# Performance work log

Hardware: AMD Instinct MI355X
Metric: run time of the kernel (lower is better)

## Reference

```python
import jax, jax.numpy as jnp
import numpy as np

N_QUBITS = 4
Q_LAYERS = 3
BATCH = 16384


def setup_inputs() -> dict:
    key = jax.random.key(0)
    ks = jax.random.split(key, 12)

    def n(k, shape, s=0.1):
        return (s * jax.random.normal(k, shape)).astype(jnp.float32)

    return {
        "x": jax.random.normal(ks[0], (BATCH, 1, 28, 28), jnp.float32),
        "conv1_w": n(ks[1], (6, 1, 5, 5)),
        "conv1_b": n(ks[2], (6,)),
        "conv2_w": n(ks[3], (16, 6, 5, 5)),
        "conv2_b": n(ks[4], (16,)),
        "fc1_w": n(ks[5], (120, 256)),
        "fc1_b": n(ks[6], (120,)),
        "fc2_w": n(ks[7], (N_QUBITS, 120)),
        "fc2_b": n(ks[8], (N_QUBITS,)),
        "q_weights": n(ks[9], (Q_LAYERS, 1, N_QUBITS, 3), 0.01),
        "clf_w": n(ks[10], (10, N_QUBITS)),
        "clf_b": n(ks[11], (10,)),
    }


def _apply_1q(state, U, w):
    # state: (B, 2,2,2,2); U: (2,2) shared or (B,2,2) per-sample
    s = jnp.moveaxis(state, 1 + w, -1)
    if U.ndim == 2:
        s = jnp.einsum('ij,...j->...i', U, s)
    else:
        s = jnp.einsum('bij,b...j->b...i', U, s)
    return jnp.moveaxis(s, -1, 1 + w)


def _cnot(state, c, t):
    s = jnp.moveaxis(state, (1 + c, 1 + t), (-2, -1))
    s = jnp.concatenate([s[..., 0:1, :], s[..., 1:2, ::-1]], axis=-2)
    return jnp.moveaxis(s, (-2, -1), (1 + c, 1 + t))


def _rot(phi, theta, omega):
    # PennyLane Rot = RZ(omega) @ RY(theta) @ RZ(phi)
    c = jnp.cos(theta / 2)
    s = jnp.sin(theta / 2)
    m00 = jnp.exp(-0.5j * (phi + omega)) * c
    m01 = -jnp.exp(0.5j * (phi - omega)) * s
    m10 = jnp.exp(0.5j * (omega - phi)) * s
    m11 = jnp.exp(0.5j * (phi + omega)) * c
    return jnp.stack([jnp.stack([m00, m01]), jnp.stack([m10, m11])])


def _rx(a):
    # a: (B,) -> (B,2,2) RX matrices
    c = jnp.cos(a / 2) + 0j
    z = -1j * jnp.sin(a / 2)
    return jnp.stack([jnp.stack([c, z], -1), jnp.stack([z, c], -1)], -2)


def _circuit(angles, qw):
    # Data-reuploading circuit: per block, StronglyEntanglingLayers(1 sublayer, r=1)
    # then AngleEmbedding (RX). Returns <Z_i> per qubit, shape (B, 4).
    Bn = angles.shape[0]
    state = jnp.zeros((Bn, 16), jnp.complex64).at[:, 0].set(1.0)
    state = state.reshape(Bn, 2, 2, 2, 2)
    n_layers = qw.shape[0]
    for l in range(n_layers):
        for w in range(N_QUBITS):
            state = _apply_1q(state, _rot(qw[l, 0, w, 0], qw[l, 0, w, 1], qw[l, 0, w, 2]), w)
        for w in range(N_QUBITS):
            state = _cnot(state, w, (w + 1) % N_QUBITS)
        for w in range(N_QUBITS):
            state = _apply_1q(state, _rx(angles[:, w]), w)
    probs = jnp.abs(state) ** 2
    z = []
    for w in range(N_QUBITS):
        p = jnp.moveaxis(probs, 1 + w, -1).reshape(Bn, -1, 2)
        z.append(p[..., 0].sum(-1) - p[..., 1].sum(-1))
    return jnp.stack(z, axis=1).astype(jnp.float32)


def _conv(x, w, b):
    y = jax.lax.conv_general_dilated(x, w, (1, 1), 'VALID',
                                     dimension_numbers=('NCHW', 'OIHW', 'NCHW'))
    return y + b[None, :, None, None]


def _pool(x):
    return jax.lax.reduce_window(x, -jnp.inf, jax.lax.max,
                                 (1, 1, 2, 2), (1, 1, 2, 2), 'VALID')


def reference(x, conv1_w, conv1_b, conv2_w, conv2_b, fc1_w, fc1_b,
              fc2_w, fc2_b, q_weights, clf_w, clf_b):
    h = _pool(jax.nn.relu(_conv(x, conv1_w, conv1_b)))       # (B,6,12,12)
    h = _pool(jax.nn.relu(_conv(h, conv2_w, conv2_b)))       # (B,16,4,4)
    h = h.reshape(h.shape[0], -1)                            # (B,256)
    h = jax.nn.relu(h @ fc1_w.T + fc1_b)                     # (B,120)
    feat = h @ fc2_w.T + fc2_b                               # (B,4)
    angles = jnp.pi * jax.nn.sigmoid(feat)
    q_out = _circuit(angles, q_weights)                      # (B,4)
    logits = q_out @ clf_w.T + clf_b                         # (B,10)
    return logits
```

## Files before the change

kernel.cpp:

```cpp
#include <hip/hip_runtime.h>
#include <math.h>

#define BATCH_N 16384

typedef _Float16 half8 __attribute__((ext_vector_type(8)));
typedef __fp16 h2 __attribute__((ext_vector_type(2)));
typedef float f32x4 __attribute__((ext_vector_type(4)));

#define C1P_F  0
#define BS1_F  120
#define BS2_F  128
#define FC2W_F 144
#define ROTM_F 628
#define RXCS_F 724
#define CWB_F  852
#define W2B_F  904
#define PW_F   2760
#define LDS_FLOATS 9768

#define WV_STRIDE_H 3504
#define H1_SAMP 1240
#define H2_OFF  2480

__global__ __launch_bounds__(256, 4) void fused_model(
    const float* __restrict__ xg,
    const float* __restrict__ c1w, const float* __restrict__ c1b,
    const float* __restrict__ c2w, const float* __restrict__ c2b,
    const float* __restrict__ f1w, const float* __restrict__ f1b,
    const float* __restrict__ f2w, const float* __restrict__ f2b,
    const float* __restrict__ qw,  const float* __restrict__ cw,
    const float* __restrict__ cbias, float* __restrict__ out) {
    __shared__ float L[LDS_FLOATS];
    const int tid = threadIdx.x;
    const int b0 = blockIdx.x * 16;
    const int lane = tid & 63, wvi = tid >> 6;
    const int ml = lane & 15, q = lane >> 4;

    _Float16* W2BH = (_Float16*)(L + W2B_F);
    _Float16* PWH  = (_Float16*)(L + PW_F);
    _Float16* H1CH = PWH + wvi * WV_STRIDE_H;
    _Float16* H2H  = H1CH + H2_OFF;
    _Float16* HSH  = (_Float16*)(L + W2B_F);

    if (tid < 120) {
        const int oc = tid / 20, r = tid - oc * 20, ky = r >> 2, j = r & 3;
        const float* wb = c1w + oc * 25 + ky * 5;
        float lo, hi;
        if (j == 0)      { lo = wb[0]; hi = wb[1]; }
        else if (j == 1) { lo = wb[2]; hi = wb[3]; }
        else if (j == 2) { lo = wb[4]; hi = 0.f;   }
        else             { lo = 0.f;   hi = wb[4]; }
        ((h2*)&L[C1P_F])[tid] = __builtin_amdgcn_cvt_pkrtz(lo, hi);
    }
    if (tid < 6)  L[BS1_F + tid] = c1b[tid];
    if (tid < 16) L[BS2_F + tid] = c2b[tid];
    for (int i = tid; i < 480; i += 256) L[FC2W_F + i] = f2w[i];
    if (tid < 4) L[FC2W_F + 480 + tid] = f2b[tid];
    if (tid < 40) L[CWB_F + tid] = cw[tid];
    if (tid < 10) L[CWB_F + 40 + tid] = cbias[tid];
    if (tid < 12) {
        const float phi = qw[tid * 3 + 0];
        const float th  = qw[tid * 3 + 1];
        const float om  = qw[tid * 3 + 2];
        const float ct = cosf(0.5f * th), st = sinf(0.5f * th);
        const float ap = 0.5f * (phi + om), bm = 0.5f * (phi - om);
        const float ca = cosf(ap), sa = sinf(ap);
        const float cbm = cosf(bm), sbm = sinf(bm);
        float* R = &L[ROTM_F + tid * 8];
        R[0] =  ct * ca;  R[1] = -ct * sa;
        R[2] = -st * cbm; R[3] = -st * sbm;
        R[4] =  st * cbm; R[5] = -st * sbm;
        R[6] =  ct * ca;  R[7] =  ct * sa;
    }
    for (int i = tid; i < 3712; i += 256) {
        const int oc = i / 232, r = i - oc * 232;
        float v = 0.f;
        if (r < 200) {
            const int pix = r >> 3, ic = r & 7;
            if (ic < 6) v = c2w[oc * 150 + ic * 25 + pix];
        }
        W2BH[oc * 232 + r] = (_Float16)v;
    }
    __syncthreads();

#pragma unroll 1
    for (int p = 0; p < 2; ++p) {
        const int sbase = b0 + 4 * wvi + 2 * p;

        for (int t = lane; t < 288; t += 64) {
            const int s = t >= 144 ? 1 : 0;
            const int r = t - s * 144;
            const int py = r / 12, px = r - (r / 12) * 12;
            const float* xp = xg + (size_t)(sbase + s) * 784 + (2 * py) * 28 + 2 * px;

            float4 X4[6]; float2 X2[6];
#pragma unroll
            for (int rr = 0; rr < 6; rr++) {
                X4[rr] = *(const float4*)(xp + rr * 28);
                X2[rr] = *(const float2*)(xp + rr * 28 + 4);
            }

            float acc[6][4];
#pragma unroll
            for (int oc = 0; oc < 6; oc++) {
                const float bv = L[BS1_F + oc];
                acc[oc][0] = bv; acc[oc][1] = bv; acc[oc][2] = bv; acc[oc][3] = bv;
            }

            h2 R0[5], R1[5];
            R0[0] = __builtin_amdgcn_cvt_pkrtz(X4[0].x, X4[0].y);
            R0[1] = __builtin_amdgcn_cvt_pkrtz(X4[0].z, X4[0].w);
            R0[2] = __builtin_amdgcn_cvt_pkrtz(X2[0].x, X2[0].y);
            R0[3] = __builtin_amdgcn_cvt_pkrtz(X4[0].y, X4[0].z);
            R0[4] = __builtin_amdgcn_cvt_pkrtz(X4[0].w, X2[0].x);
#pragma unroll
            for (int ky = 0; ky < 5; ky++) {
                R1[0] = __builtin_amdgcn_cvt_pkrtz(X4[ky + 1].x, X4[ky + 1].y);
                R1[1] = __builtin_amdgcn_cvt_pkrtz(X4[ky + 1].z, X4[ky + 1].w);
                R1[2] = __builtin_amdgcn_cvt_pkrtz(X2[ky + 1].x, X2[ky + 1].y);
                R1[3] = __builtin_amdgcn_cvt_pkrtz(X4[ky + 1].y, X4[ky + 1].z);
                R1[4] = __builtin_amdgcn_cvt_pkrtz(X4[ky + 1].w, X2[ky + 1].x);
#pragma unroll
                for (int oc = 0; oc < 6; oc++) {
                    union { uint4 v; h2 h[4]; } W;
                    W.v = ((const uint4*)&L[C1P_F])[oc * 5 + ky];
                    acc[oc][0] = __builtin_amdgcn_fdot2(R0[0], W.h[0], acc[oc][0], false);
                    acc[oc][0] = __builtin_amdgcn_fdot2(R0[1], W.h[1], acc[oc][0], false);
                    acc[oc][0] = __builtin_amdgcn_fdot2(R0[2], W.h[2], acc[oc][0], false);
                    acc[oc][1] = __builtin_amdgcn_fdot2(R0[3], W.h[0], acc[oc][1], false);
                    acc[oc][1] = __builtin_amdgcn_fdot2(R0[4], W.h[1], acc[oc][1], false);
                    acc[oc][1] = __builtin_amdgcn_fdot2(R0[2], W.h[3], acc[oc][1], false);
                    acc[oc][2] = __builtin_amdgcn_fdot2(R1[0], W.h[0], acc[oc][2], false);
                    acc[oc][2] = __builtin_amdgcn_fdot2(R1[1], W.h[1], acc[oc][2], false);
                    acc[oc][2] = __builtin_amdgcn_fdot2(R1[2], W.h[2], acc[oc][2], false);
                    acc[oc][3] = __builtin_amdgcn_fdot2(R1[3], W.h[0], acc[oc][3], false);
                    acc[oc][3] = __builtin_amdgcn_fdot2(R1[4], W.h[1], acc[oc][3], false);
                    acc[oc][3] = __builtin_amdgcn_fdot2(R1[2], W.h[3], acc[oc][3], false);
                }
#pragma unroll
                for (int j = 0; j < 5; j++) R0[j] = R1[j];
            }

            union { _Float16 h[8]; uint4 u; } O;
#pragma unroll
            for (int oc = 0; oc < 6; oc++) {
                const float m = fmaxf(fmaxf(acc[oc][0], acc[oc][1]), fmaxf(acc[oc][2], acc[oc][3]));
                O.h[oc] = (_Float16)fmaxf(m, 0.f);
            }
            O.h[6] = (_Float16)0.f; O.h[7] = (_Float16)0.f;
            *(uint4*)(H1CH + s * H1_SAMP + (py * 13 + px) * 8) = O.u;
        }
        __builtin_amdgcn_wave_barrier();

        {
            f32x4 c2a[2][4];
#pragma unroll
            for (int a = 0; a < 2; a++)
#pragma unroll
                for (int b = 0; b < 4; b++) c2a[a][b] = (f32x4){0.f, 0.f, 0.f, 0.f};

#pragma unroll
            for (int ks = 0; ks < 7; ks++) {
                const half8 bfrag = *(const half8*)(W2BH + ml * 232 + ks * 32 + q * 8);
                int tp = ks * 4 + q; if (tp > 24) tp = 24;
                const int poff = (tp / 5) * 13 + (tp % 5);
#pragma unroll
                for (int si = 0; si < 2; si++) {
                    const _Float16* hp = H1CH + si * H1_SAMP;
#pragma unroll
                    for (int t = 0; t < 4; t++) {
                        const int cp = t * 16 + ml;
                        const int unit = (cp >> 3) * 13 + (cp & 7) + poff;
                        const half8 afrag = *(const half8*)(hp + unit * 8);
                        c2a[si][t] = __builtin_amdgcn_mfma_f32_16x16x32_f16(afrag, bfrag, c2a[si][t], 0, 0, 0);
                    }
                }
            }

            const float bv = L[BS2_F + ml];
#pragma unroll
            for (int si = 0; si < 2; si++) {
#pragma unroll
                for (int t = 0; t < 4; t++) {
                    const float c0 = c2a[si][t][0] + bv, c1 = c2a[si][t][1] + bv;
                    const float c2 = c2a[si][t][2] + bv, c3 = c2a[si][t][3] + bv;
                    float px0 = fmaxf(c0, c1), px1 = fmaxf(c2, c3);
                    px0 = fmaxf(px0, __shfl_xor(px0, 32));
                    px1 = fmaxf(px1, __shfl_xor(px1, 32));
                    if (lane < 32) {
                        union { _Float16 h[2]; unsigned u; } P2;
                        P2.h[0] = (_Float16)fmaxf(px0, 0.f);
                        P2.h[1] = (_Float16)fmaxf(px1, 0.f);
                        *(unsigned*)(H2H + (2 * p + si) * 256 + ml * 16 + t * 4 + (q & 1) * 2) = P2.u;
                    }
                }
            }
        }
        __builtin_amdgcn_wave_barrier();
    }
    __syncthreads();

    {
        f32x4 fcC[2];
        fcC[0] = (f32x4){0.f, 0.f, 0.f, 0.f};
        fcC[1] = (f32x4){0.f, 0.f, 0.f, 0.f};
        const _Float16* h2p = PWH + (ml >> 2) * WV_STRIDE_H + H2_OFF + (ml & 3) * 256;
#pragma unroll
        for (int ks = 0; ks < 8; ks++) {
            const half8 afrag = *(const half8*)(h2p + ks * 32 + q * 8);
#pragma unroll
            for (int ti = 0; ti < 2; ti++) {
                const int n = (wvi + 4 * ti) * 16 + ml;
                half8 bfrag;
                if (n < 120) {
                    const float* wp = f1w + (size_t)n * 256 + ks * 32 + q * 8;
                    const float4 u = *(const float4*)wp;
                    const float4 v = *(const float4*)(wp + 4);
                    bfrag[0] = (_Float16)u.x; bfrag[1] = (_Float16)u.y;
                    bfrag[2] = (_Float16)u.z; bfrag[3] = (_Float16)u.w;
                    bfrag[4] = (_Float16)v.x; bfrag[5] = (_Float16)v.y;
                    bfrag[6] = (_Float16)v.z; bfrag[7] = (_Float16)v.w;
                } else {
#pragma unroll
                    for (int j = 0; j < 8; j++) bfrag[j] = (_Float16)0.f;
                }
                fcC[ti] = __builtin_amdgcn_mfma_f32_16x16x32_f16(afrag, bfrag, fcC[ti], 0, 0, 0);
            }
        }
#pragma unroll
        for (int ti = 0; ti < 2; ti++) {
            const int n = (wvi + 4 * ti) * 16 + ml;
            if (n < 120) {
                const float bb = f1b[n];
#pragma unroll
                for (int rg = 0; rg < 4; rg++) {
                    const int s = q * 4 + rg;
                    HSH[s * 128 + n] = (_Float16)fmaxf(fcC[ti][rg] + bb, 0.f);
                }
            }
        }
    }
    __syncthreads();

    if (tid < 64) {
        const int s = tid >> 2, m = tid & 3;
        float f = L[FC2W_F + 480 + m];
        for (int nn = 0; nn < 120; nn += 8) {
            const half8 hv = *(const half8*)(HSH + s * 128 + nn);
            const float* wp = &L[FC2W_F + m * 120 + nn];
            f = fmaf(wp[0], (float)hv[0], f); f = fmaf(wp[1], (float)hv[1], f);
            f = fmaf(wp[2], (float)hv[2], f); f = fmaf(wp[3], (float)hv[3], f);
            f = fmaf(wp[4], (float)hv[4], f); f = fmaf(wp[5], (float)hv[5], f);
            f = fmaf(wp[6], (float)hv[6], f); f = fmaf(wp[7], (float)hv[7], f);
        }
        const float ang = 3.14159265358979323846f / (1.f + expf(-f));
        L[RXCS_F + tid]      = cosf(0.5f * ang);
        L[RXCS_F + 64 + tid] = sinf(0.5f * ang);
    }
    __syncthreads();

    {
        const int s = tid >> 4, a = tid & 15;
        float ar = (a == 0) ? 1.f : 0.f, ai = 0.f;

#pragma unroll
        for (int l = 0; l < 3; l++) {
#pragma unroll
            for (int w = 0; w < 4; w++) {
                const float* R = &L[ROTM_F + (l * 4 + w) * 8];
                const int mask = 8 >> w;
                const float pr = __shfl_xor(ar, mask);
                const float pi = __shfl_xor(ai, mask);
                const bool bit = (a & mask) != 0;
                const float lr = bit ? pr : ar, li = bit ? pi : ai;
                const float hr = bit ? ar : pr, hi = bit ? ai : pi;
                const float Ar = bit ? R[4] : R[0], Ai = bit ? R[5] : R[1];
                const float Br = bit ? R[6] : R[2], Bi = bit ? R[7] : R[3];
                ar = Ar * lr - Ai * li + Br * hr - Bi * hi;
                ai = Ar * li + Ai * lr + Br * hi + Bi * hr;
            }
#pragma unroll
            for (int w = 0; w < 4; w++) {
                const int mc = 8 >> w, mt = 8 >> ((w + 1) & 3);
                const float pr = __shfl_xor(ar, mt);
                const float pi = __shfl_xor(ai, mt);
                const bool ctrl = (a & mc) != 0;
                ar = ctrl ? pr : ar;
                ai = ctrl ? pi : ai;
            }
#pragma unroll
            for (int w = 0; w < 4; w++) {
                const int mask = 8 >> w;
                const float c  = L[RXCS_F + s * 4 + w];
                const float s2 = L[RXCS_F + 64 + s * 4 + w];
                const float pr = __shfl_xor(ar, mask);
                const float pi = __shfl_xor(ai, mask);
                const float nr = fmaf(c, ar, s2 * pi);
                const float ni = fmaf(c, ai, -s2 * pr);
                ar = nr; ai = ni;
            }
        }

        float v = ar * ar + ai * ai;
#pragma unroll
        for (int d = 1; d < 16; d <<= 1) {
            const float pv = __shfl_xor(v, d);
            v = (a & d) ? (pv - v) : (v + pv);
        }

        if (a < 10) {
            const int base = (tid & 63) & ~15;
            float lg = L[CWB_F + 40 + a];
#pragma unroll
            for (int w = 0; w < 4; w++) {
                const float zw = __shfl(v, base | (8 >> w));
                lg = fmaf(L[CWB_F + a * 4 + w], zw, lg);
            }
            out[(size_t)(b0 + s) * 10 + a] = lg;
        }
    }
}

extern "C" void kernel_launch(void* const* d_in, const int* in_sizes, int n_in,
                              void* d_out, int out_size, void* d_ws, size_t ws_size,
                              hipStream_t stream) {
    const float* x   = (const float*)d_in[0];
    const float* c1w = (const float*)d_in[1];
    const float* c1b = (const float*)d_in[2];
    const float* c2w = (const float*)d_in[3];
    const float* c2b = (const float*)d_in[4];
    const float* f1w = (const float*)d_in[5];
    const float* f1b = (const float*)d_in[6];
    const float* f2w = (const float*)d_in[7];
    const float* f2b = (const float*)d_in[8];
    const float* qw  = (const float*)d_in[9];
    const float* cw  = (const float*)d_in[10];
    const float* cb  = (const float*)d_in[11];
    float* out = (float*)d_out;

    fused_model<<<BATCH_N / 16, 256, 0, stream>>>(x, c1w, c1b, c2w, c2b,
                                                  f1w, f1b, f2w, f2b,
                                                  qw, cw, cb, out);
}
```

Before: 157.3 us.

## Stage input tile in LDS as fp16, hold pooled conv2 in registers, spread fc2

Each wave now loads its two 28x28 input images once, coalesced, into LDS as packed fp16. The conv1 taps are then read from LDS with shifted unsigned words, replacing six overlapping float4/float2 global loads per thread. Pooled conv2 outputs stay in registers until a block barrier and are then written to a compact shared A-matrix for fc1. fc2 is split across all 256 threads with shuffle reductions and reads its weights directly from global memory. Other changes include incremental index math for the conv2 weight staging, packed fp16 conversions for the fc1 weights, and a reorganised LDS layout. The cost is a larger LDS footprint and more registers, which may reduce occupancy.

```diff
diff --git a/kernel.cpp b/kernel.cpp
--- a/kernel.cpp
+++ b/kernel.cpp
@@ -10,17 +10,34 @@
 #define C1P_F  0
 #define BS1_F  120
 #define BS2_F  128
-#define FC2W_F 144
-#define ROTM_F 628
-#define RXCS_F 724
-#define CWB_F  852
-#define W2B_F  904
-#define PW_F   2760
-#define LDS_FLOATS 9768
-
-#define WV_STRIDE_H 3504
-#define H1_SAMP 1240
-#define H2_OFF  2480
+#define ROTM_F 144
+#define RXCS_F 240
+#define CWB_F  368
+#define W2B_F  420
+#define PW_F   2276
+#define LDS_FLOATS 10020
+
+#define WV_STRIDE_H 3872
+#define XH_SAMP_H   784
+#define H1_OFF_H    1568
+#define H1_SAMP_H   1152
+#define H2A_ROW_H   264
+#define HS_OFF_H    4224
+#define HS_ROW_H    136
+
+static __device__ __forceinline__ h2 u2h(unsigned u) {
+    union { unsigned u; h2 h; } c; c.u = u; return c.h;
+}
+
+struct Row5 { h2 a0, a1, a2, s0, s1; };
+static __device__ __forceinline__ Row5 ldrow(const unsigned* xw) {
+    const unsigned u0 = xw[0], u1 = xw[1], u2 = xw[2];
+    Row5 r;
+    r.a0 = u2h(u0); r.a1 = u2h(u1); r.a2 = u2h(u2);
+    r.s0 = u2h((u0 >> 16) | (u1 << 16));
+    r.s1 = u2h((u1 >> 16) | (u2 << 16));
+    return r;
+}
 
 __global__ __launch_bounds__(256, 4) void fused_model(
     const float* __restrict__ xg,
@@ -38,9 +55,10 @@
 
     _Float16* W2BH = (_Float16*)(L + W2B_F);
     _Float16* PWH  = (_Float16*)(L + PW_F);
-    _Float16* H1CH = PWH + wvi * WV_STRIDE_H;
-    _Float16* H2H  = H1CH + H2_OFF;
-    _Float16* HSH  = (_Float16*)(L + W2B_F);
+    _Float16* XHH  = PWH + wvi * WV_STRIDE_H;
+    _Float16* H1CH = XHH + H1_OFF_H;
+    _Float16* H2AH = PWH;
+    _Float16* HSH  = PWH + HS_OFF_H;
 
     if (tid < 120) {
         const int oc = tid / 20, r = tid - oc * 20, ky = r >> 2, j = r & 3;
@@ -54,8 +72,6 @@
     }
     if (tid < 6)  L[BS1_F + tid] = c1b[tid];
     if (tid < 16) L[BS2_F + tid] = c2b[tid];
-    for (int i = tid; i < 480; i += 256) L[FC2W_F + i] = f2w[i];
-    if (tid < 4) L[FC2W_F + 480 + tid] = f2b[tid];
     if (tid < 40) L[CWB_F + tid] = cw[tid];
     if (tid < 10) L[CWB_F + 40 + tid] = cbias[tid];
     if (tid < 12) {
@@ -72,33 +88,46 @@
         R[4] =  st * cbm; R[5] = -st * sbm;
         R[6] =  ct * ca;  R[7] =  ct * sa;
     }
-    for (int i = tid; i < 3712; i += 256) {
-        const int oc = i / 232, r = i - oc * 232;
-        float v = 0.f;
-        if (r < 200) {
-            const int pix = r >> 3, ic = r & 7;
-            if (ic < 6) v = c2w[oc * 150 + ic * 25 + pix];
-        }
-        W2BH[oc * 232 + r] = (_Float16)v;
-    }
-    __syncthreads();
-
+    {
+        int oc = (tid >= 232) ? 1 : 0;
+        int r = tid - oc * 232;
 #pragma unroll 1
+        for (int i = tid; i < 3712; i += 256) {
+            float v = 0.f;
+            if (r < 200) {
+                const int pix = r >> 3, ic = r & 7;
+                if (ic < 6) v = c2w[oc * 150 + ic * 25 + pix];
+            }
+            W2BH[oc * 232 + r] = (_Float16)v;
+            r += 24; oc += 1;
+            if (r >= 232) { r -= 232; oc += 1; }
+        }
+    }
+    __syncthreads();
+
+    unsigned h2r[2][2][4];
+
+#pragma unroll 2
     for (int p = 0; p < 2; ++p) {
         const int sbase = b0 + 4 * wvi + 2 * p;
+
+        for (int k = lane; k < 392; k += 64) {
+            const int s = (k >= 196) ? 1 : 0;
+            const int kk = k - 196 * s;
+            const int row = kk / 7, q4 = kk - row * 7;
+            const float4 v = *(const float4*)(xg + (size_t)(sbase + s) * 784 + row * 28 + q4 * 4);
+            union { h2 h[2]; uint2 u; } W;
+            W.h[0] = __builtin_amdgcn_cvt_pkrtz(v.x, v.y);
+            W.h[1] = __builtin_amdgcn_cvt_pkrtz(v.z, v.w);
+            *(uint2*)(XHH + s * XH_SAMP_H + row * 28 + q4 * 4) = W.u;
+        }
+        __builtin_amdgcn_wave_barrier();
 
         for (int t = lane; t < 288; t += 64) {
             const int s = t >= 144 ? 1 : 0;
             const int r = t - s * 144;
             const int py = r / 12, px = r - (r / 12) * 12;
-            const float* xp = xg + (size_t)(sbase + s) * 784 + (2 * py) * 28 + 2 * px;
-
-            float4 X4[6]; float2 X2[6];
-#pragma unroll
-            for (int rr = 0; rr < 6; rr++) {
-                X4[rr] = *(const float4*)(xp + rr * 28);
-                X2[rr] = *(const float2*)(xp + rr * 28 + 4);
-            }
+            const unsigned* xw = (const unsigned*)(XHH + s * XH_SAMP_H) + 2 * py * 14 + px;
 
             float acc[6][4];
 #pragma unroll
@@ -107,38 +136,28 @@
                 acc[oc][0] = bv; acc[oc][1] = bv; acc[oc][2] = bv; acc[oc][3] = bv;
             }
 
-            h2 R0[5], R1[5];
-            R0[0] = __builtin_amdgcn_cvt_pkrtz(X4[0].x, X4[0].y);
-            R0[1] = __builtin_amdgcn_cvt_pkrtz(X4[0].z, X4[0].w);
-            R0[2] = __builtin_amdgcn_cvt_pkrtz(X2[0].x, X2[0].y);
-            R0[3] = __builtin_amdgcn_cvt_pkrtz(X4[0].y, X4[0].z);
-            R0[4] = __builtin_amdgcn_cvt_pkrtz(X4[0].w, X2[0].x);
+            Row5 R0 = ldrow(xw);
 #pragma unroll
             for (int ky = 0; ky < 5; ky++) {
-                R1[0] = __builtin_amdgcn_cvt_pkrtz(X4[ky + 1].x, X4[ky + 1].y);
-                R1[1] = __builtin_amdgcn_cvt_pkrtz(X4[ky + 1].z, X4[ky + 1].w);
-                R1[2] = __builtin_amdgcn_cvt_pkrtz(X2[ky + 1].x, X2[ky + 1].y);
-                R1[3] = __builtin_amdgcn_cvt_pkrtz(X4[ky + 1].y, X4[ky + 1].z);
-                R1[4] = __builtin_amdgcn_cvt_pkrtz(X4[ky + 1].w, X2[ky + 1].x);
+                const Row5 R1 = ldrow(xw + (ky + 1) * 14);
 #pragma unroll
                 for (int oc = 0; oc < 6; oc++) {
                     union { uint4 v; h2 h[4]; } W;
                     W.v = ((const uint4*)&L[C1P_F])[oc * 5 + ky];
-                    acc[oc][0] = __builtin_amdgcn_fdot2(R0[0], W.h[0], acc[oc][0], false);
-                    acc[oc][0] = __builtin_amdgcn_fdot2(R0[1], W.h[1], acc[oc][0], false);
-                    acc[oc][0] = __builtin_amdgcn_fdot2(R0[2], W.h[2], acc[oc][0], false);
-                    acc[oc][1] = __builtin_amdgcn_fdot2(R0[3], W.h[0], acc[oc][1], false);
-                    acc[oc][1] = __builtin_amdgcn_fdot2(R0[4], W.h[1], acc[oc][1], false);
-                    acc[oc][1] = __builtin_amdgcn_fdot2(R0[2], W.h[3], acc[oc][1], false);
-                    acc[oc][2] = __builtin_amdgcn_fdot2(R1[0], W.h[0], acc[oc][2], false);
-                    acc[oc][2] = __builtin_amdgcn_fdot2(R1[1], W.h[1], acc[oc][2], false);
-                    acc[oc][2] = __builtin_amdgcn_fdot2(R1[2], W.h[2], acc[oc][2], false);
-                    acc[oc][3] = __builtin_amdgcn_fdot2(R1[3], W.h[0], acc[oc][3], false);
-                    acc[oc][3] = __builtin_amdgcn_fdot2(R1[4], W.h[1], acc[oc][3], false);
-                    acc[oc][3] = __builtin_amdgcn_fdot2(R1[2], W.h[3], acc[oc][3], false);
-                }
-#pragma unroll
-                for (int j = 0; j < 5; j++) R0[j] = R1[j];
+                    acc[oc][0] = __builtin_amdgcn_fdot2(R0.a0, W.h[0], acc[oc][0], false);
+                    acc[oc][0] = __builtin_amdgcn_fdot2(R0.a1, W.h[1], acc[oc][0], false);
+                    acc[oc][0] = __builtin_amdgcn_fdot2(R0.a2, W.h[2], acc[oc][0], false);
+                    acc[oc][1] = __builtin_amdgcn_fdot2(R0.s0, W.h[0], acc[oc][1], false);
+                    acc[oc][1] = __builtin_amdgcn_fdot2(R0.s1, W.h[1], acc[oc][1], false);
+                    acc[oc][1] = __builtin_amdgcn_fdot2(R0.a2, W.h[3], acc[oc][1], false);
+                    acc[oc][2] = __builtin_amdgcn_fdot2(R1.a0, W.h[0], acc[oc][2], false);
+                    acc[oc][2] = __builtin_amdgcn_fdot2(R1.a1, W.h[1], acc[oc][2], false);
+                    acc[oc][2] = __builtin_amdgcn_fdot2(R1.a2, W.h[2], acc[oc][2], false);
+                    acc[oc][3] = __builtin_amdgcn_fdot2(R1.s0, W.h[0], acc[oc][3], false);
+                    acc[oc][3] = __builtin_amdgcn_fdot2(R1.s1, W.h[1], acc[oc][3], false);
+                    acc[oc][3] = __builtin_amdgcn_fdot2(R1.a2, W.h[3], acc[oc][3], false);
+                }
+                R0 = R1;
             }
 
             union { _Float16 h[8]; uint4 u; } O;
@@ -148,7 +167,7 @@
                 O.h[oc] = (_Float16)fmaxf(m, 0.f);
             }
             O.h[6] = (_Float16)0.f; O.h[7] = (_Float16)0.f;
-            *(uint4*)(H1CH + s * H1_SAMP + (py * 13 + px) * 8) = O.u;
+            *(uint4*)(H1CH + s * H1_SAMP_H + (py * 12 + px) * 8) = O.u;
         }
         __builtin_amdgcn_wave_barrier();
 
@@ -163,14 +182,14 @@
             for (int ks = 0; ks < 7; ks++) {
                 const half8 bfrag = *(const half8*)(W2BH + ml * 232 + ks * 32 + q * 8);
                 int tp = ks * 4 + q; if (tp > 24) tp = 24;
-                const int poff = (tp / 5) * 13 + (tp % 5);
+                const int poff = (tp / 5) * 12 + (tp % 5);
 #pragma unroll
                 for (int si = 0; si < 2; si++) {
-                    const _Float16* hp = H1CH + si * H1_SAMP;
+                    const _Float16* hp = H1CH + si * H1_SAMP_H;
 #pragma unroll
                     for (int t = 0; t < 4; t++) {
                         const int cp = t * 16 + ml;
-                        const int unit = (cp >> 3) * 13 + (cp & 7) + poff;
+                        const int unit = (cp >> 3) * 12 + (cp & 7) + poff;
                         const half8 afrag = *(const half8*)(hp + unit * 8);
                         c2a[si][t] = __builtin_amdgcn_mfma_f32_16x16x32_f16(afrag, bfrag, c2a[si][t], 0, 0, 0);
                     }
@@ -187,16 +206,27 @@
                     float px0 = fmaxf(c0, c1), px1 = fmaxf(c2, c3);
                     px0 = fmaxf(px0, __shfl_xor(px0, 32));
                     px1 = fmaxf(px1, __shfl_xor(px1, 32));
-                    if (lane < 32) {
-                        union { _Float16 h[2]; unsigned u; } P2;
-                        P2.h[0] = (_Float16)fmaxf(px0, 0.f);
-                        P2.h[1] = (_Float16)fmaxf(px1, 0.f);
-                        *(unsigned*)(H2H + (2 * p + si) * 256 + ml * 16 + t * 4 + (q & 1) * 2) = P2.u;
-                    }
+                    union { _Float16 h[2]; unsigned u; } P2;
+                    P2.h[0] = (_Float16)fmaxf(px0, 0.f);
+                    P2.h[1] = (_Float16)fmaxf(px1, 0.f);
+                    h2r[p][si][t] = P2.u;
                 }
             }
         }
         __builtin_amdgcn_wave_barrier();
+    }
+    __syncthreads();
+
+    if (lane < 32) {
+#pragma unroll
+        for (int p = 0; p < 2; p++)
+#pragma unroll
+            for (int si = 0; si < 2; si++)
+#pragma unroll
+                for (int t = 0; t < 4; t++) {
+                    const int srow = 4 * wvi + 2 * p + si;
+                    *(unsigned*)(H2AH + srow * H2A_ROW_H + ml * 16 + t * 4 + q * 2) = h2r[p][si][t];
+                }
     }
     __syncthreads();
 
@@ -204,7 +234,7 @@
         f32x4 fcC[2];
         fcC[0] = (f32x4){0.f, 0.f, 0.f, 0.f};
         fcC[1] = (f32x4){0.f, 0.f, 0.f, 0.f};
-        const _Float16* h2p = PWH + (ml >> 2) * WV_STRIDE_H + H2_OFF + (ml & 3) * 256;
+        const _Float16* h2p = H2AH + ml * H2A_ROW_H;
 #pragma unroll
         for (int ks = 0; ks < 8; ks++) {
             const half8 afrag = *(const half8*)(h2p + ks * 32 + q * 8);
@@ -216,10 +246,12 @@
                     const float* wp = f1w + (size_t)n * 256 + ks * 32 + q * 8;
                     const float4 u = *(const float4*)wp;
                     const float4 v = *(const float4*)(wp + 4);
-                    bfrag[0] = (_Float16)u.x; bfrag[1] = (_Float16)u.y;
-                    bfrag[2] = (_Float16)u.z; bfrag[3] = (_Float16)u.w;
-                    bfrag[4] = (_Float16)v.x; bfrag[5] = (_Float16)v.y;
-                    bfrag[6] = (_Float16)v.z; bfrag[7] = (_Float16)v.w;
+                    union { h2 p[4]; half8 h8; } B;
+                    B.p[0] = __builtin_amdgcn_cvt_pkrtz(u.x, u.y);
+                    B.p[1] = __builtin_amdgcn_cvt_pkrtz(u.z, u.w);
+                    B.p[2] = __builtin_amdgcn_cvt_pkrtz(v.x, v.y);
+                    B.p[3] = __builtin_amdgcn_cvt_pkrtz(v.z, v.w);
+                    bfrag = B.h8;
                 } else {
 #pragma unroll
                     for (int j = 0; j < 8; j++) bfrag[j] = (_Float16)0.f;
@@ -235,27 +267,37 @@
 #pragma unroll
                 for (int rg = 0; rg < 4; rg++) {
                     const int s = q * 4 + rg;
-                    HSH[s * 128 + n] = (_Float16)fmaxf(fcC[ti][rg] + bb, 0.f);
-                }
-            }
-        }
-    }
-    __syncthreads();
-
-    if (tid < 64) {
-        const int s = tid >> 2, m = tid & 3;
-        float f = L[FC2W_F + 480 + m];
-        for (int nn = 0; nn < 120; nn += 8) {
-            const half8 hv = *(const half8*)(HSH + s * 128 + nn);
-            const float* wp = &L[FC2W_F + m * 120 + nn];
-            f = fmaf(wp[0], (float)hv[0], f); f = fmaf(wp[1], (float)hv[1], f);
-            f = fmaf(wp[2], (float)hv[2], f); f = fmaf(wp[3], (float)hv[3], f);
-            f = fmaf(wp[4], (float)hv[4], f); f = fmaf(wp[5], (float)hv[5], f);
-            f = fmaf(wp[6], (float)hv[6], f); f = fmaf(wp[7], (float)hv[7], f);
-        }
-        const float ang = 3.14159265358979323846f / (1.f + expf(-f));
-        L[RXCS_F + tid]      = cosf(0.5f * ang);
-        L[RXCS_F + 64 + tid] = sinf(0.5f * ang);
+                    HSH[s * HS_ROW_H + n] = (_Float16)fmaxf(fcC[ti][rg] + bb, 0.f);
+                }
+            }
+        }
+    }
+    __syncthreads();
+
+    {
+        const int s = tid >> 4, m = (tid >> 2) & 3, part = tid & 3;
+        float f = (part == 0) ? f2b[m] : 0.f;
+#pragma unroll
+        for (int i = 0; i < 4; ++i) {
+            const int bblk = part + 4 * i;
+            if (bblk < 15) {
+                const half8 hv = *(const half8*)(HSH + s * HS_ROW_H + bblk * 8);
+                const float* wp = f2w + m * 120 + bblk * 8;
+                const float4 w0 = *(const float4*)wp;
+                const float4 w1 = *(const float4*)(wp + 4);
+                f = fmaf(w0.x, (float)hv[0], f); f = fmaf(w0.y, (float)hv[1], f);
+                f = fmaf(w0.z, (float)hv[2], f); f = fmaf(w0.w, (float)hv[3], f);
+                f = fmaf(w1.x, (float)hv[4], f); f = fmaf(w1.y, (float)hv[5], f);
+                f = fmaf(w1.z, (float)hv[6], f); f = fmaf(w1.w, (float)hv[7], f);
+            }
+        }
+        f += __shfl_xor(f, 1);
+        f += __shfl_xor(f, 2);
+        if (part == 0) {
+            const float ang = 3.14159265358979323846f / (1.f + expf(-f));
+            L[RXCS_F + s * 4 + m]      = cosf(0.5f * ang);
+            L[RXCS_F + 64 + s * 4 + m] = sinf(0.5f * ang);
+        }
     }
     __syncthreads();
 
```

Result: slower. 162.5 us (+3.3%).
